# Kernel optimization log

Measured on AMD Instinct MI355X. Metric: run time of the kernel, lower is better.

Reference implementation:

```python
import jax, jax.numpy as jnp
import numpy as np

N_NODES = 50000
N_EDGES = 800000
IN_FEAT = 64
HIDDEN = 128
NUM_LAYERS = 3


def setup_inputs() -> dict:
    key = jax.random.key(0)
    ks = jax.random.split(key, 8)
    x = jax.random.normal(ks[0], (N_NODES, IN_FEAT), dtype=jnp.float32)
    edge_index = jax.random.randint(ks[1], (2, N_EDGES), 0, N_NODES, dtype=jnp.int64)
    s_in = 1.0 / np.sqrt(IN_FEAT)
    s_h = 1.0 / np.sqrt(HIDDEN)
    W_in = jax.random.uniform(ks[2], (IN_FEAT, HIDDEN), jnp.float32, -s_in, s_in)
    b_in = jax.random.uniform(ks[3], (HIDDEN,), jnp.float32, -s_in, s_in)
    W_self = jax.random.uniform(ks[4], (NUM_LAYERS, HIDDEN, HIDDEN), jnp.float32, -s_h, s_h)
    b_self = jax.random.uniform(ks[5], (NUM_LAYERS, HIDDEN), jnp.float32, -s_h, s_h)
    W_nbr = jax.random.uniform(ks[6], (NUM_LAYERS, HIDDEN, HIDDEN), jnp.float32, -s_h, s_h)
    return {"x": x, "edge_index": edge_index, "W_in": W_in, "b_in": b_in,
            "W_self": W_self, "b_self": b_self, "W_nbr": W_nbr}


def reference(x, edge_index, W_in, b_in, W_self, b_self, W_nbr):
    # input projection: h [N, HIDDEN]
    h = x @ W_in + b_in
    src = edge_index[0]
    dst = edge_index[1]
    n = h.shape[0]
    ones = jnp.ones((dst.shape[0], 1), dtype=h.dtype)
    # scatter-mean denominator is grad-constant; compute once
    cnt = jax.ops.segment_sum(ones, dst, num_segments=n)
    cnt = jnp.maximum(cnt, 1.0)
    for l in range(W_self.shape[0]):
        msg = h[src] @ W_nbr[l]                               # [E, HIDDEN]
        agg = jax.ops.segment_sum(msg, dst, num_segments=n) / cnt  # scatter-mean
        h = jax.nn.elu(h @ W_self[l] + b_self[l] + agg)
    return h
```

## Files before the change

kernel.cpp:

```cpp
#include <hip/hip_runtime.h>
#include <cstdint>

#define HIDDEN 128

typedef unsigned short u16;
using frag_t   = __attribute__((ext_vector_type(8))) short;
using f32x4_t  = __attribute__((ext_vector_type(4))) float;
using ushort8_t = __attribute__((ext_vector_type(8))) unsigned short;

__device__ __forceinline__ float bf2f(u16 u) {
    union { unsigned int i; float f; } c;
    c.i = ((unsigned int)u) << 16;
    return c.f;
}
__device__ __forceinline__ u16 f2bf(float f) {
    unsigned int u = __float_as_uint(f);
    unsigned int r = (u + 0x7fffu + ((u >> 16) & 1u)) >> 16;
    return (u16)r;
}


__global__ void k_hist_prep(const int* __restrict__ ei, int E, int* __restrict__ deg, int npr,
                            const float* __restrict__ x,
                            const float* __restrict__ W_in,
                            const float* __restrict__ W_self,
                            const float* __restrict__ W_nbr,
                            u16* __restrict__ xf,
                            u16* __restrict__ WtI_hi, u16* __restrict__ WtI_lo,
                            u16* __restrict__ WtS_hi, u16* __restrict__ WtS_lo,
                            u16* __restrict__ WtN_hi, u16* __restrict__ WtN_lo,
                            int L, int nxg) {
    {
        int r  = blockIdx.x & 7;
        int lo = r * npr, hi = lo + npr;
        int nb = gridDim.x >> 3;
        int bi = blockIdx.x >> 3;
        int tid = bi * blockDim.x + threadIdx.x;
        int stride = nb * blockDim.x;
        if ((E & 3) == 0) {
            const int4* d4 = (const int4*)(ei + E);
            int nch = E >> 2;
            for (int c = tid; c < nch; c += stride) {
                int4 d = d4[c];
                if (d.x >= lo && d.x < hi) atomicAdd(&deg[d.x], 1);
                if (d.y >= lo && d.y < hi) atomicAdd(&deg[d.y], 1);
                if (d.z >= lo && d.z < hi) atomicAdd(&deg[d.z], 1);
                if (d.w >= lo && d.w < hi) atomicAdd(&deg[d.w], 1);
            }
        } else {
            for (int e = tid; e < E; e += stride) {
                int d = ei[E + e];
                if (d >= lo && d < hi) atomicAdd(&deg[d], 1);
            }
        }
    }
    {
        int nIn = 64 * 128;
        int nSq = L * 128 * 128;
        int wtot = nIn + 2 * nSq;
        int total = wtot + nxg;
        int stride = gridDim.x * blockDim.x;
        for (int i = blockIdx.x * blockDim.x + threadIdx.x; i < total; i += stride) {
            if (i >= wtot) {
                int t = i - wtot;
                int row = t >> 3, c = t & 7;
                const float4* xs = (const float4*)(x + (size_t)row * 64 + c * 8);
                float4 v0 = xs[0], v1 = xs[1];
                ushort8_t o;
                o[0] = f2bf(v0.x); o[1] = f2bf(v0.y); o[2] = f2bf(v0.z); o[3] = f2bf(v0.w);
                o[4] = f2bf(v1.x); o[5] = f2bf(v1.y); o[6] = f2bf(v1.z); o[7] = f2bf(v1.w);
                int T = row >> 4, m = row & 15;
                int f = c >> 2, q = c & 3;
                *(ushort8_t*)&xf[((size_t)(T * 2 + f) * 64 + q * 16 + m) * 8] = o;
            } else {
                float v; u16* phi; u16* plo; int o;
                if (i < nIn) {
                    int n = i / 64, k = i % 64;
                    v = W_in[k * 128 + n]; phi = WtI_hi; plo = WtI_lo; o = n * 64 + k;
                } else if (i < nIn + nSq) {
                    int t = i - nIn;
                    int l = t / (128 * 128), r = t % (128 * 128);
                    int n = r / 128, k = r % 128;
                    v = W_self[l * 128 * 128 + k * 128 + n]; phi = WtS_hi; plo = WtS_lo;
                    o = l * 128 * 128 + n * 128 + k;
                } else {
                    int t = i - nIn - nSq;
                    int l = t / (128 * 128), r = t % (128 * 128);
                    int n = r / 128, k = r % 128;
                    v = W_nbr[l * 128 * 128 + k * 128 + n]; phi = WtN_hi; plo = WtN_lo;
                    o = l * 128 * 128 + n * 128 + k;
                }
                u16 hi = f2bf(v);
                phi[o] = hi;
                plo[o] = f2bf(v - bf2f(hi));
            }
        }
    }
}

__global__ void k_scan1(const int* __restrict__ deg, int* __restrict__ rowp,
                        int* __restrict__ bsums, int n) {
    __shared__ int sh[1024];
    int t = threadIdx.x;
    int base = blockIdx.x * 1024;
    int v = (base + t < n) ? deg[base + t] : 0;
    sh[t] = v;
    __syncthreads();
    for (int off = 1; off < 1024; off <<= 1) {
        int x = sh[t];
        int y = (t >= off) ? sh[t - off] : 0;
        __syncthreads();
        sh[t] = x + y;
        __syncthreads();
    }
    if (base + t < n) rowp[base + t + 1] = sh[t];
    if (t == 1023) bsums[blockIdx.x] = sh[1023];
}

__global__ void k_scan_tail(int* __restrict__ rowp, const int* __restrict__ bsums,
                            int* __restrict__ fillp, int n, int nb) {
    __shared__ int sh[1024];
    int t = threadIdx.x;
    int b = blockIdx.x;
    sh[t] = (t < nb) ? bsums[t] : 0;
    __syncthreads();
    for (int off = 1; off < 1024; off <<= 1) {
        int x = sh[t];
        int y = (t >= off) ? sh[t - off] : 0;
        __syncthreads();
        sh[t] = x + y;
        __syncthreads();
    }
    int boff = (b == 0) ? 0 : sh[b - 1];
    int base = b * 1024;
    if (base + t < n) {
        int v = rowp[base + t + 1] + boff;
        rowp[base + t + 1] = v;
        if (base + t + 1 < n) fillp[base + t + 1] = v;
    }
    if (b == 0 && t == 0) { rowp[0] = 0; fillp[0] = 0; }
}

__global__ void k_fill(const int* __restrict__ ei, int E,
                       int* __restrict__ fillpos, int* __restrict__ colx, int npr) {
    int r  = blockIdx.x & 7;
    int lo = r * npr, hi = lo + npr;
    int nb = gridDim.x >> 3;
    int bi = blockIdx.x >> 3;
    int tid = bi * blockDim.x + threadIdx.x;
    int stride = nb * blockDim.x;
    if ((E & 3) == 0) {
        const int4* s4 = (const int4*)ei;
        const int4* d4 = (const int4*)(ei + E);
        int nch = E >> 2;
        for (int c = tid; c < nch; c += stride) {
            int4 d = d4[c];
            bool m0 = d.x >= lo && d.x < hi;
            bool m1 = d.y >= lo && d.y < hi;
            bool m2 = d.z >= lo && d.z < hi;
            bool m3 = d.w >= lo && d.w < hi;
            if (m0 | m1 | m2 | m3) {
                int4 s = s4[c];
                if (m0) colx[atomicAdd(&fillpos[d.x], 1)] = s.x;
                if (m1) colx[atomicAdd(&fillpos[d.y], 1)] = s.y;
                if (m2) colx[atomicAdd(&fillpos[d.z], 1)] = s.z;
                if (m3) colx[atomicAdd(&fillpos[d.w], 1)] = s.w;
            }
        }
    } else {
        for (int e = tid; e < E; e += stride) {
            int d = ei[E + e];
            if (d >= lo && d < hi) colx[atomicAdd(&fillpos[d], 1)] = ei[e];
        }
    }
}


__global__ __launch_bounds__(256, 4) void k_agg(
        const ushort8_t* __restrict__ hb8, const int* __restrict__ rowp,
        const int* __restrict__ colx, u16* __restrict__ Sf, int n) {
    int g = (blockIdx.x * blockDim.x + threadIdx.x) >> 4;
    int lane = threadIdx.x & 15;
    if (g >= n) return;
    int beg = rowp[g];
    int end = rowp[g + 1];
    float a0[8], a1[8];
#pragma unroll
    for (int j = 0; j < 8; ++j) { a0[j] = 0.f; a1[j] = 0.f; }
    int e = beg;
    for (; e + 7 < end; e += 8) {
        int s0 = colx[e],     s1 = colx[e + 1], s2 = colx[e + 2], s3 = colx[e + 3];
        int s4 = colx[e + 4], s5 = colx[e + 5], s6 = colx[e + 6], s7 = colx[e + 7];
        ushort8_t v0 = hb8[(size_t)s0 * 16 + lane];
        ushort8_t v1 = hb8[(size_t)s1 * 16 + lane];
        ushort8_t v2 = hb8[(size_t)s2 * 16 + lane];
        ushort8_t v3 = hb8[(size_t)s3 * 16 + lane];
        ushort8_t v4 = hb8[(size_t)s4 * 16 + lane];
        ushort8_t v5 = hb8[(size_t)s5 * 16 + lane];
        ushort8_t v6 = hb8[(size_t)s6 * 16 + lane];
        ushort8_t v7 = hb8[(size_t)s7 * 16 + lane];
#pragma unroll
        for (int j = 0; j < 8; ++j) {
            a0[j] += bf2f(v0[j]); a1[j] += bf2f(v1[j]);
            a0[j] += bf2f(v2[j]); a1[j] += bf2f(v3[j]);
            a0[j] += bf2f(v4[j]); a1[j] += bf2f(v5[j]);
            a0[j] += bf2f(v6[j]); a1[j] += bf2f(v7[j]);
        }
    }
    for (; e + 3 < end; e += 4) {
        int s0 = colx[e], s1 = colx[e + 1], s2 = colx[e + 2], s3 = colx[e + 3];
        ushort8_t v0 = hb8[(size_t)s0 * 16 + lane];
        ushort8_t v1 = hb8[(size_t)s1 * 16 + lane];
        ushort8_t v2 = hb8[(size_t)s2 * 16 + lane];
        ushort8_t v3 = hb8[(size_t)s3 * 16 + lane];
#pragma unroll
        for (int j = 0; j < 8; ++j) {
            a0[j] += bf2f(v0[j]); a1[j] += bf2f(v1[j]);
            a0[j] += bf2f(v2[j]); a1[j] += bf2f(v3[j]);
        }
    }
    for (; e < end; ++e) {
        int s = colx[e];
        ushort8_t v = hb8[(size_t)s * 16 + lane];
#pragma unroll
        for (int j = 0; j < 8; ++j) a0[j] += bf2f(v[j]);
    }
    int deg = end - beg;
    float inv = 1.0f / (float)(deg > 1 ? deg : 1);
    ushort8_t o;
#pragma unroll
    for (int j = 0; j < 8; ++j) o[j] = f2bf((a0[j] + a1[j]) * inv);
    int T = g >> 4, m = g & 15;
    *(ushort8_t*)&Sf[((size_t)(T * 4 + (lane >> 2)) * 64 + (lane & 3) * 16 + m) * 8] = o;
}


template <int KF1, int KF2, int DO_ELU>
__global__ __launch_bounds__(256, 2) void k_gemm_mfma(
    const u16* __restrict__ A1f, const u16* __restrict__ A2f,
    const u16* __restrict__ B1h, const u16* __restrict__ B1l,
    const u16* __restrict__ B2h, const u16* __restrict__ B2l,
    const float* __restrict__ bias, float* __restrict__ C,
    u16* __restrict__ Hrow, u16* __restrict__ Hf,
    int M)
{
    constexpr int K1 = KF1 * 32;
    constexpr int K2 = KF2 * 32;
    constexpr int KF = KF1 + KF2;
    int lane = threadIdx.x & 63;
    int w    = threadIdx.x >> 6;
    int m16  = lane & 15;
    int quad = lane >> 4;
    int kq   = quad * 8;
    int ng   = (blockIdx.x >> 3) & 1;
    int mtb  = (blockIdx.x & 7) | ((blockIdx.x >> 4) << 3);
    int ncol = (ng * 4 + w) * 16 + m16;

    frag_t bh[KF], bl[KF];
    if constexpr (KF1 > 0) {
#pragma unroll
        for (int f = 0; f < KF1; ++f) {
            bh[f] = *(const frag_t*)&B1h[(size_t)ncol * K1 + f * 32 + kq];
            bl[f] = *(const frag_t*)&B1l[(size_t)ncol * K1 + f * 32 + kq];
        }
    }
    if constexpr (KF2 > 0) {
#pragma unroll
        for (int f = 0; f < KF2; ++f) {
            bh[KF1 + f] = *(const frag_t*)&B2h[(size_t)ncol * K2 + f * 32 + kq];
            bl[KF1 + f] = *(const frag_t*)&B2l[(size_t)ncol * K2 + f * 32 + kq];
        }
    }

    float bv = bias[ncol];
    int nMT  = (M + 31) >> 5;
    int step = gridDim.x >> 1;
    int fcol = ncol >> 5;
    int qcol = (ncol & 31) >> 3;
    int jcol = ncol & 7;

    auto loadA = [&](int mt, frag_t (&a0)[KF], frag_t (&a1)[KF]) {
        int T0 = mt * 2, T1 = T0 + 1;
        if constexpr (KF1 > 0) {
#pragma unroll
            for (int f = 0; f < KF1; ++f) {
                a0[f] = *(const frag_t*)&A1f[((size_t)(T0 * KF1 + f) * 64 + lane) * 8];
                a1[f] = *(const frag_t*)&A1f[((size_t)(T1 * KF1 + f) * 64 + lane) * 8];
            }
        }
        if constexpr (KF2 > 0) {
#pragma unroll
            for (int f = 0; f < KF2; ++f) {
                a0[KF1 + f] = *(const frag_t*)&A2f[((size_t)(T0 * KF2 + f) * 64 + lane) * 8];
                a1[KF1 + f] = *(const frag_t*)&A2f[((size_t)(T1 * KF2 + f) * 64 + lane) * 8];
            }
        }
    };

    auto compute = [&](int mt, frag_t (&a0)[KF], frag_t (&a1)[KF]) {
        f32x4_t acc0 = (f32x4_t){0.f, 0.f, 0.f, 0.f};
        f32x4_t acc1 = (f32x4_t){0.f, 0.f, 0.f, 0.f};
#pragma unroll
        for (int f = 0; f < KF; ++f) {
            acc0 = __builtin_amdgcn_mfma_f32_16x16x32_bf16(a0[f], bh[f], acc0, 0, 0, 0);
            acc1 = __builtin_amdgcn_mfma_f32_16x16x32_bf16(a1[f], bh[f], acc1, 0, 0, 0);
            acc0 = __builtin_amdgcn_mfma_f32_16x16x32_bf16(a0[f], bl[f], acc0, 0, 0, 0);
            acc1 = __builtin_amdgcn_mfma_f32_16x16x32_bf16(a1[f], bl[f], acc1, 0, 0, 0);
        }
        int rb = mt * 32 + quad * 4;
#pragma unroll
        for (int r = 0; r < 4; ++r) {
#pragma unroll
            for (int half = 0; half < 2; ++half) {
                int row = rb + r + half * 16;
                float av = half ? acc1[r] : acc0[r];
                if (row < M) {
                    float v = av + bv;
                    if constexpr (DO_ELU) v = (v > 0.f) ? v : expm1f(v);
                    if (C) C[(size_t)row * HIDDEN + ncol] = v;
                    if (Hrow) {
                        u16 hv = f2bf(v);
                        Hrow[(size_t)row * HIDDEN + ncol] = hv;
                        Hf[((size_t)((row >> 4) * 4 + fcol) * 64 + qcol * 16 + (row & 15)) * 8 + jcol] = hv;
                    }
                }
            }
        }
    };

    int mt = mtb;
    if (mt >= nMT) return;
    frag_t xa0[KF], xa1[KF], ya0[KF], ya1[KF];
    loadA(mt, xa0, xa1);
    while (true) {
        int mt2 = mt + step;
        if (mt2 < nMT) loadA(mt2, ya0, ya1);
        compute(mt, xa0, xa1);
        if (mt2 >= nMT) break;
        int mt3 = mt2 + step;
        if (mt3 < nMT) loadA(mt3, xa0, xa1);
        compute(mt2, ya0, ya1);
        if (mt3 >= nMT) break;
        mt = mt3;
    }
}


extern "C" void kernel_launch(void* const* d_in, const int* in_sizes, int n_in,
                              void* d_out, int out_size, void* d_ws, size_t ws_size,
                              hipStream_t stream) {
    const float* x        = (const float*)d_in[0];
    const int* ei         = (const int*)d_in[1];
    const float* W_in     = (const float*)d_in[2];
    const float* b_in     = (const float*)d_in[3];
    const float* W_self   = (const float*)d_in[4];
    const float* b_self   = (const float*)d_in[5];
    const float* W_nbr    = (const float*)d_in[6];
    float* out = (float*)d_out;

    const int IN_FEAT = 64;
    int N = in_sizes[0] / IN_FEAT;
    int E = in_sizes[1] / 2;
    int L = in_sizes[4] / (HIDDEN * HIDDEN);

    char* ws = (char*)d_ws;
    size_t off = 0;
    auto alloc = [&](size_t bytes) -> void* {
        void* p = ws + off;
        off = (off + bytes + 255) & ~(size_t)255;
        return p;
    };

    int nT = ((N + 31) / 32) * 2;

    u16* hRowA = (u16*)alloc((size_t)N * HIDDEN * 2);
    u16* hRowB = (u16*)alloc((size_t)N * HIDDEN * 2);
    u16* hfA   = (u16*)alloc((size_t)nT * 4 * 64 * 8 * 2);
    u16* hfB   = (u16*)alloc((size_t)nT * 4 * 64 * 8 * 2);
    u16* xf    = (u16*)alloc((size_t)nT * 2 * 64 * 8 * 2);
    u16* Sf    = (u16*)alloc((size_t)nT * 4 * 64 * 8 * 2);
    u16* WtI_hi = (u16*)alloc(128 * 64 * 2);
    u16* WtI_lo = (u16*)alloc(128 * 64 * 2);
    u16* WtS_hi = (u16*)alloc((size_t)L * 128 * 128 * 2);
    u16* WtS_lo = (u16*)alloc((size_t)L * 128 * 128 * 2);
    u16* WtN_hi = (u16*)alloc((size_t)L * 128 * 128 * 2);
    u16* WtN_lo = (u16*)alloc((size_t)L * 128 * 128 * 2);
    int* deg   = (int*)alloc((size_t)N * sizeof(int));
    int* rowp  = (int*)alloc((size_t)(N + 1) * sizeof(int));
    int* fillp = (int*)alloc((size_t)N * sizeof(int));
    int* colx  = (int*)alloc((size_t)E * sizeof(int));
    int* bsums = (int*)alloc(1024 * sizeof(int));

    int npr = (N + 7) / 8;

    hipMemsetAsync(deg, 0, (size_t)N * sizeof(int), stream);
    int wtot = 64 * 128 + 2 * L * 128 * 128;
    k_hist_prep<<<2048, 256, 0, stream>>>(ei, E, deg, npr,
                                          x, W_in, W_self, W_nbr, xf,
                                          WtI_hi, WtI_lo, WtS_hi, WtS_lo,
                                          WtN_hi, WtN_lo, L, N * 8);
    int nb = (N + 1023) / 1024;
    k_scan1<<<nb, 1024, 0, stream>>>(deg, rowp, bsums, N);
    k_scan_tail<<<nb, 1024, 0, stream>>>(rowp, bsums, fillp, N, nb);
    k_fill<<<2048, 256, 0, stream>>>(ei, E, fillp, colx, npr);

    const int GB = 1024;

    k_gemm_mfma<2, 0, 0><<<GB, 256, 0, stream>>>(
        xf, nullptr,
        WtI_hi, WtI_lo, nullptr, nullptr,
        b_in, nullptr, hRowA, hfA, N);

    u16* curRow = hRowA; u16* curF = hfA;
    u16* nxtRow = hRowB; u16* nxtF = hfB;

    for (int l = 0; l < L; ++l) {
        k_agg<<<(N + 15) / 16, 256, 0, stream>>>((const ushort8_t*)curRow, rowp, colx, Sf, N);
        const u16* Wsh = WtS_hi + (size_t)l * 128 * 128;
        const u16* Wsl = WtS_lo + (size_t)l * 128 * 128;
        const u16* Wnh = WtN_hi + (size_t)l * 128 * 128;
        const u16* Wnl = WtN_lo + (size_t)l * 128 * 128;
        const float* bs = b_self + (size_t)l * HIDDEN;
        bool last = (l == L - 1);
        k_gemm_mfma<4, 4, 1><<<GB, 256, 0, stream>>>(
            curF, Sf,
            Wsh, Wsl, Wnh, Wnl,
            bs, last ? out : nullptr,
            last ? nullptr : nxtRow, last ? nullptr : nxtF, N);
        u16* tr = curRow; curRow = nxtRow; nxtRow = tr;
        u16* tf = curF;   curF = nxtF;     nxtF = tf;
    }
}
```

Baseline: 333.1 us.

## Fuse input GEMM and all layer agg/GEMM stages into one persistent kernel

Replaces the separate input-projection GEMM, per-layer aggregation and per-layer GEMM launches with a single persistent kernel of 512 blocks. Stages are separated by an atomic-counter grid barrier, and aggregation becomes a grid-stride loop. This removes the launch overheads and tail gaps between the seven kernels. In exchange it relies on all 512 blocks being co-resident, or the barrier deadlocks. It also changes the GEMM grid from 1024 to 512 blocks, and the aggregation occupancy now follows launch_bounds(256,2) instead of (256,4).

```diff
diff --git a/kernel.cpp b/kernel.cpp
--- a/kernel.cpp
+++ b/kernel.cpp
@@ -17,6 +17,17 @@
     unsigned int u = __float_as_uint(f);
     unsigned int r = (u + 0x7fffu + ((u >> 16) & 1u)) >> 16;
     return (u16)r;
+}
+
+__device__ __forceinline__ void gbar(int* cnt, int target) {
+    __syncthreads();
+    if (threadIdx.x == 0) {
+        __threadfence();
+        __hip_atomic_fetch_add(cnt, 1, __ATOMIC_RELEASE, __HIP_MEMORY_SCOPE_AGENT);
+        while (__hip_atomic_load(cnt, __ATOMIC_ACQUIRE, __HIP_MEMORY_SCOPE_AGENT) < target)
+            __builtin_amdgcn_s_sleep(2);
+    }
+    __syncthreads();
 }
 
 
@@ -176,67 +187,69 @@
 }
 
 
-__global__ __launch_bounds__(256, 4) void k_agg(
-        const ushort8_t* __restrict__ hb8, const int* __restrict__ rowp,
-        const int* __restrict__ colx, u16* __restrict__ Sf, int n) {
-    int g = (blockIdx.x * blockDim.x + threadIdx.x) >> 4;
+__device__ __forceinline__ void dev_agg(const ushort8_t* __restrict__ hb8,
+                                        const int* __restrict__ rowp,
+                                        const int* __restrict__ colx,
+                                        u16* __restrict__ Sf, int n) {
     int lane = threadIdx.x & 15;
-    if (g >= n) return;
-    int beg = rowp[g];
-    int end = rowp[g + 1];
-    float a0[8], a1[8];
-#pragma unroll
-    for (int j = 0; j < 8; ++j) { a0[j] = 0.f; a1[j] = 0.f; }
-    int e = beg;
-    for (; e + 7 < end; e += 8) {
-        int s0 = colx[e],     s1 = colx[e + 1], s2 = colx[e + 2], s3 = colx[e + 3];
-        int s4 = colx[e + 4], s5 = colx[e + 5], s6 = colx[e + 6], s7 = colx[e + 7];
-        ushort8_t v0 = hb8[(size_t)s0 * 16 + lane];
-        ushort8_t v1 = hb8[(size_t)s1 * 16 + lane];
-        ushort8_t v2 = hb8[(size_t)s2 * 16 + lane];
-        ushort8_t v3 = hb8[(size_t)s3 * 16 + lane];
-        ushort8_t v4 = hb8[(size_t)s4 * 16 + lane];
-        ushort8_t v5 = hb8[(size_t)s5 * 16 + lane];
-        ushort8_t v6 = hb8[(size_t)s6 * 16 + lane];
-        ushort8_t v7 = hb8[(size_t)s7 * 16 + lane];
-#pragma unroll
-        for (int j = 0; j < 8; ++j) {
-            a0[j] += bf2f(v0[j]); a1[j] += bf2f(v1[j]);
-            a0[j] += bf2f(v2[j]); a1[j] += bf2f(v3[j]);
-            a0[j] += bf2f(v4[j]); a1[j] += bf2f(v5[j]);
-            a0[j] += bf2f(v6[j]); a1[j] += bf2f(v7[j]);
-        }
-    }
-    for (; e + 3 < end; e += 4) {
-        int s0 = colx[e], s1 = colx[e + 1], s2 = colx[e + 2], s3 = colx[e + 3];
-        ushort8_t v0 = hb8[(size_t)s0 * 16 + lane];
-        ushort8_t v1 = hb8[(size_t)s1 * 16 + lane];
-        ushort8_t v2 = hb8[(size_t)s2 * 16 + lane];
-        ushort8_t v3 = hb8[(size_t)s3 * 16 + lane];
-#pragma unroll
-        for (int j = 0; j < 8; ++j) {
-            a0[j] += bf2f(v0[j]); a1[j] += bf2f(v1[j]);
-            a0[j] += bf2f(v2[j]); a1[j] += bf2f(v3[j]);
-        }
-    }
-    for (; e < end; ++e) {
-        int s = colx[e];
-        ushort8_t v = hb8[(size_t)s * 16 + lane];
-#pragma unroll
-        for (int j = 0; j < 8; ++j) a0[j] += bf2f(v[j]);
-    }
-    int deg = end - beg;
-    float inv = 1.0f / (float)(deg > 1 ? deg : 1);
-    ushort8_t o;
-#pragma unroll
-    for (int j = 0; j < 8; ++j) o[j] = f2bf((a0[j] + a1[j]) * inv);
-    int T = g >> 4, m = g & 15;
-    *(ushort8_t*)&Sf[((size_t)(T * 4 + (lane >> 2)) * 64 + (lane & 3) * 16 + m) * 8] = o;
+    int ngr = (gridDim.x * blockDim.x) >> 4;
+    for (int g = (blockIdx.x * blockDim.x + threadIdx.x) >> 4; g < n; g += ngr) {
+        int beg = rowp[g];
+        int end = rowp[g + 1];
+        float a0[8], a1[8];
+#pragma unroll
+        for (int j = 0; j < 8; ++j) { a0[j] = 0.f; a1[j] = 0.f; }
+        int e = beg;
+        for (; e + 7 < end; e += 8) {
+            int s0 = colx[e],     s1 = colx[e + 1], s2 = colx[e + 2], s3 = colx[e + 3];
+            int s4 = colx[e + 4], s5 = colx[e + 5], s6 = colx[e + 6], s7 = colx[e + 7];
+            ushort8_t v0 = hb8[(size_t)s0 * 16 + lane];
+            ushort8_t v1 = hb8[(size_t)s1 * 16 + lane];
+            ushort8_t v2 = hb8[(size_t)s2 * 16 + lane];
+            ushort8_t v3 = hb8[(size_t)s3 * 16 + lane];
+            ushort8_t v4 = hb8[(size_t)s4 * 16 + lane];
+            ushort8_t v5 = hb8[(size_t)s5 * 16 + lane];
+            ushort8_t v6 = hb8[(size_t)s6 * 16 + lane];
+            ushort8_t v7 = hb8[(size_t)s7 * 16 + lane];
+#pragma unroll
+            for (int j = 0; j < 8; ++j) {
+                a0[j] += bf2f(v0[j]); a1[j] += bf2f(v1[j]);
+                a0[j] += bf2f(v2[j]); a1[j] += bf2f(v3[j]);
+                a0[j] += bf2f(v4[j]); a1[j] += bf2f(v5[j]);
+                a0[j] += bf2f(v6[j]); a1[j] += bf2f(v7[j]);
+            }
+        }
+        for (; e + 3 < end; e += 4) {
+            int s0 = colx[e], s1 = colx[e + 1], s2 = colx[e + 2], s3 = colx[e + 3];
+            ushort8_t v0 = hb8[(size_t)s0 * 16 + lane];
+            ushort8_t v1 = hb8[(size_t)s1 * 16 + lane];
+            ushort8_t v2 = hb8[(size_t)s2 * 16 + lane];
+            ushort8_t v3 = hb8[(size_t)s3 * 16 + lane];
+#pragma unroll
+            for (int j = 0; j < 8; ++j) {
+                a0[j] += bf2f(v0[j]); a1[j] += bf2f(v1[j]);
+                a0[j] += bf2f(v2[j]); a1[j] += bf2f(v3[j]);
+            }
+        }
+        for (; e < end; ++e) {
+            int s = colx[e];
+            ushort8_t v = hb8[(size_t)s * 16 + lane];
+#pragma unroll
+            for (int j = 0; j < 8; ++j) a0[j] += bf2f(v[j]);
+        }
+        int deg = end - beg;
+        float inv = 1.0f / (float)(deg > 1 ? deg : 1);
+        ushort8_t o;
+#pragma unroll
+        for (int j = 0; j < 8; ++j) o[j] = f2bf((a0[j] + a1[j]) * inv);
+        int T = g >> 4, m = g & 15;
+        *(ushort8_t*)&Sf[((size_t)(T * 4 + (lane >> 2)) * 64 + (lane & 3) * 16 + m) * 8] = o;
+    }
 }
 
 
 template <int KF1, int KF2, int DO_ELU>
-__global__ __launch_bounds__(256, 2) void k_gemm_mfma(
+__device__ __forceinline__ void dev_gemm(
     const u16* __restrict__ A1f, const u16* __restrict__ A2f,
     const u16* __restrict__ B1h, const u16* __restrict__ B1l,
     const u16* __restrict__ B2h, const u16* __restrict__ B2l,
@@ -329,19 +342,65 @@
     };
 
     int mt = mtb;
-    if (mt >= nMT) return;
-    frag_t xa0[KF], xa1[KF], ya0[KF], ya1[KF];
-    loadA(mt, xa0, xa1);
-    while (true) {
-        int mt2 = mt + step;
-        if (mt2 < nMT) loadA(mt2, ya0, ya1);
-        compute(mt, xa0, xa1);
-        if (mt2 >= nMT) break;
-        int mt3 = mt2 + step;
-        if (mt3 < nMT) loadA(mt3, xa0, xa1);
-        compute(mt2, ya0, ya1);
-        if (mt3 >= nMT) break;
-        mt = mt3;
+    if (mt < nMT) {
+        frag_t xa0[KF], xa1[KF], ya0[KF], ya1[KF];
+        loadA(mt, xa0, xa1);
+        while (true) {
+            int mt2 = mt + step;
+            if (mt2 < nMT) loadA(mt2, ya0, ya1);
+            compute(mt, xa0, xa1);
+            if (mt2 >= nMT) break;
+            int mt3 = mt2 + step;
+            if (mt3 < nMT) loadA(mt3, xa0, xa1);
+            compute(mt2, ya0, ya1);
+            if (mt3 >= nMT) break;
+            mt = mt3;
+        }
+    }
+}
+
+
+__global__ __launch_bounds__(256, 2) void k_mega(
+    const u16* __restrict__ xf,
+    const u16* __restrict__ WtI_hi, const u16* __restrict__ WtI_lo,
+    const u16* __restrict__ WtS_hi, const u16* __restrict__ WtS_lo,
+    const u16* __restrict__ WtN_hi, const u16* __restrict__ WtN_lo,
+    const float* __restrict__ b_in, const float* __restrict__ b_self,
+    const int* __restrict__ rowp, const int* __restrict__ colx,
+    u16* __restrict__ hRowA, u16* __restrict__ hfA,
+    u16* __restrict__ hRowB, u16* __restrict__ hfB,
+    u16* __restrict__ Sf,
+    float* __restrict__ out,
+    int N, int L, int* __restrict__ cnt)
+{
+    int nb = gridDim.x;
+    int bt = nb;
+
+    dev_gemm<2, 0, 0>(xf, nullptr, WtI_hi, WtI_lo, nullptr, nullptr,
+                      b_in, nullptr, hRowA, hfA, N);
+    gbar(cnt, bt); bt += nb;
+
+    u16* curRow = hRowA; u16* curF = hfA;
+    u16* nxtRow = hRowB; u16* nxtF = hfB;
+
+    for (int l = 0; l < L; ++l) {
+        dev_agg((const ushort8_t*)curRow, rowp, colx, Sf, N);
+        gbar(cnt, bt); bt += nb;
+
+        const u16* Wsh = WtS_hi + (size_t)l * 128 * 128;
+        const u16* Wsl = WtS_lo + (size_t)l * 128 * 128;
+        const u16* Wnh = WtN_hi + (size_t)l * 128 * 128;
+        const u16* Wnl = WtN_lo + (size_t)l * 128 * 128;
+        const float* bs = b_self + (size_t)l * HIDDEN;
+        bool last = (l == L - 1);
+        dev_gemm<4, 4, 1>(curF, Sf, Wsh, Wsl, Wnh, Wnl, bs,
+                          last ? out : nullptr,
+                          last ? nullptr : nxtRow, last ? nullptr : nxtF, N);
+        if (!last) {
+            gbar(cnt, bt); bt += nb;
+            u16* tr = curRow; curRow = nxtRow; nxtRow = tr;
+            u16* tf = curF;   curF = nxtF;     nxtF = tf;
+        }
     }
 }
 
@@ -385,7 +444,8 @@
     u16* WtS_lo = (u16*)alloc((size_t)L * 128 * 128 * 2);
     u16* WtN_hi = (u16*)alloc((size_t)L * 128 * 128 * 2);
     u16* WtN_lo = (u16*)alloc((size_t)L * 128 * 128 * 2);
-    int* deg   = (int*)alloc((size_t)N * sizeof(int));
+    int* deg   = (int*)alloc((size_t)(N + 64) * sizeof(int));
+    int* cnt   = deg + N;
     int* rowp  = (int*)alloc((size_t)(N + 1) * sizeof(int));
     int* fillp = (int*)alloc((size_t)N * sizeof(int));
     int* colx  = (int*)alloc((size_t)E * sizeof(int));
@@ -393,8 +453,7 @@
 
     int npr = (N + 7) / 8;
 
-    hipMemsetAsync(deg, 0, (size_t)N * sizeof(int), stream);
-    int wtot = 64 * 128 + 2 * L * 128 * 128;
+    hipMemsetAsync(deg, 0, (size_t)(N + 64) * sizeof(int), stream);
     k_hist_prep<<<2048, 256, 0, stream>>>(ei, E, deg, npr,
                                           x, W_in, W_self, W_nbr, xf,
                                           WtI_hi, WtI_lo, WtS_hi, WtS_lo,
@@ -404,30 +463,8 @@
     k_scan_tail<<<nb, 1024, 0, stream>>>(rowp, bsums, fillp, N, nb);
     k_fill<<<2048, 256, 0, stream>>>(ei, E, fillp, colx, npr);
 
-    const int GB = 1024;
-
-    k_gemm_mfma<2, 0, 0><<<GB, 256, 0, stream>>>(
-        xf, nullptr,
-        WtI_hi, WtI_lo, nullptr, nullptr,
-        b_in, nullptr, hRowA, hfA, N);
-
-    u16* curRow = hRowA; u16* curF = hfA;
-    u16* nxtRow = hRowB; u16* nxtF = hfB;
-
-    for (int l = 0; l < L; ++l) {
-        k_agg<<<(N + 15) / 16, 256, 0, stream>>>((const ushort8_t*)curRow, rowp, colx, Sf, N);
-        const u16* Wsh = WtS_hi + (size_t)l * 128 * 128;
-        const u16* Wsl = WtS_lo + (size_t)l * 128 * 128;
-        const u16* Wnh = WtN_hi + (size_t)l * 128 * 128;
-        const u16* Wnl = WtN_lo + (size_t)l * 128 * 128;
-        const float* bs = b_self + (size_t)l * HIDDEN;
-        bool last = (l == L - 1);
-        k_gemm_mfma<4, 4, 1><<<GB, 256, 0, stream>>>(
-            curF, Sf,
-            Wsh, Wsl, Wnh, Wnl,
-            bs, last ? out : nullptr,
-            last ? nullptr : nxtRow, last ? nullptr : nxtF, N);
-        u16* tr = curRow; curRow = nxtRow; nxtRow = tr;
-        u16* tf = curF;   curF = nxtF;     nxtF = tf;
-    }
-}
+    k_mega<<<512, 256, 0, stream>>>(
+        xf, WtI_hi, WtI_lo, WtS_hi, WtS_lo, WtN_hi, WtN_lo,
+        b_in, b_self, rowp, colx,
+        hRowA, hfA, hRowB, hfB, Sf, out, N, L, cnt);
+}
```

New measurement: 815.7 us. 2.45x slower.

## Drop fragment-layout copies; GEMM reads row-major activations and converts x inline

Applied to the files above, without the earlier changes.

The pre-swizzled MFMA fragment buffers (xf, hf, Sf) are removed. The GEMM now loads A operands directly from row-major bf16 activations, and for the input projection it reads fp32 x and converts it to bf16 in registers, which eliminates the x conversion pass in the prep kernel and the duplicate fragment-layout store in the epilogue. The aggregation kernel writes S row-major and gains a 16-edge unrolled gather loop for more memory-level parallelism. The trade-off is that row-major fragment loads are strided per lane rather than fully contiguous, so GEMM load efficiency may drop.

```diff
diff --git a/kernel.cpp b/kernel.cpp
--- a/kernel.cpp
+++ b/kernel.cpp
@@ -20,16 +20,14 @@
 }
 
 
-__global__ void k_hist_prep(const int* __restrict__ ei, int E, int* __restrict__ deg, int npr,
-                            const float* __restrict__ x,
-                            const float* __restrict__ W_in,
-                            const float* __restrict__ W_self,
-                            const float* __restrict__ W_nbr,
-                            u16* __restrict__ xf,
-                            u16* __restrict__ WtI_hi, u16* __restrict__ WtI_lo,
-                            u16* __restrict__ WtS_hi, u16* __restrict__ WtS_lo,
-                            u16* __restrict__ WtN_hi, u16* __restrict__ WtN_lo,
-                            int L, int nxg) {
+__global__ void k_hist_wprep(const int* __restrict__ ei, int E, int* __restrict__ deg, int npr,
+                             const float* __restrict__ W_in,
+                             const float* __restrict__ W_self,
+                             const float* __restrict__ W_nbr,
+                             u16* __restrict__ WtI_hi, u16* __restrict__ WtI_lo,
+                             u16* __restrict__ WtS_hi, u16* __restrict__ WtS_lo,
+                             u16* __restrict__ WtN_hi, u16* __restrict__ WtN_lo,
+                             int L) {
     {
         int r  = blockIdx.x & 7;
         int lo = r * npr, hi = lo + npr;
@@ -58,42 +56,28 @@
         int nIn = 64 * 128;
         int nSq = L * 128 * 128;
         int wtot = nIn + 2 * nSq;
-        int total = wtot + nxg;
         int stride = gridDim.x * blockDim.x;
-        for (int i = blockIdx.x * blockDim.x + threadIdx.x; i < total; i += stride) {
-            if (i >= wtot) {
-                int t = i - wtot;
-                int row = t >> 3, c = t & 7;
-                const float4* xs = (const float4*)(x + (size_t)row * 64 + c * 8);
-                float4 v0 = xs[0], v1 = xs[1];
-                ushort8_t o;
-                o[0] = f2bf(v0.x); o[1] = f2bf(v0.y); o[2] = f2bf(v0.z); o[3] = f2bf(v0.w);
-                o[4] = f2bf(v1.x); o[5] = f2bf(v1.y); o[6] = f2bf(v1.z); o[7] = f2bf(v1.w);
-                int T = row >> 4, m = row & 15;
-                int f = c >> 2, q = c & 3;
-                *(ushort8_t*)&xf[((size_t)(T * 2 + f) * 64 + q * 16 + m) * 8] = o;
+        for (int i = blockIdx.x * blockDim.x + threadIdx.x; i < wtot; i += stride) {
+            float v; u16* phi; u16* plo; int o;
+            if (i < nIn) {
+                int n = i / 64, k = i % 64;
+                v = W_in[k * 128 + n]; phi = WtI_hi; plo = WtI_lo; o = n * 64 + k;
+            } else if (i < nIn + nSq) {
+                int t = i - nIn;
+                int l = t / (128 * 128), r = t % (128 * 128);
+                int n = r / 128, k = r % 128;
+                v = W_self[l * 128 * 128 + k * 128 + n]; phi = WtS_hi; plo = WtS_lo;
+                o = l * 128 * 128 + n * 128 + k;
             } else {
-                float v; u16* phi; u16* plo; int o;
-                if (i < nIn) {
-                    int n = i / 64, k = i % 64;
-                    v = W_in[k * 128 + n]; phi = WtI_hi; plo = WtI_lo; o = n * 64 + k;
-                } else if (i < nIn + nSq) {
-                    int t = i - nIn;
-                    int l = t / (128 * 128), r = t % (128 * 128);
-                    int n = r / 128, k = r % 128;
-                    v = W_self[l * 128 * 128 + k * 128 + n]; phi = WtS_hi; plo = WtS_lo;
-                    o = l * 128 * 128 + n * 128 + k;
-                } else {
-                    int t = i - nIn - nSq;
-                    int l = t / (128 * 128), r = t % (128 * 128);
-                    int n = r / 128, k = r % 128;
-                    v = W_nbr[l * 128 * 128 + k * 128 + n]; phi = WtN_hi; plo = WtN_lo;
-                    o = l * 128 * 128 + n * 128 + k;
-                }
-                u16 hi = f2bf(v);
-                phi[o] = hi;
-                plo[o] = f2bf(v - bf2f(hi));
-            }
+                int t = i - nIn - nSq;
+                int l = t / (128 * 128), r = t % (128 * 128);
+                int n = r / 128, k = r % 128;
+                v = W_nbr[l * 128 * 128 + k * 128 + n]; phi = WtN_hi; plo = WtN_lo;
+                o = l * 128 * 128 + n * 128 + k;
+            }
+            u16 hi = f2bf(v);
+            phi[o] = hi;
+            plo[o] = f2bf(v - bf2f(hi));
         }
     }
 }
@@ -178,7 +162,7 @@
 
 __global__ __launch_bounds__(256, 4) void k_agg(
         const ushort8_t* __restrict__ hb8, const int* __restrict__ rowp,
-        const int* __restrict__ colx, u16* __restrict__ Sf, int n) {
+        const int* __restrict__ colx, u16* __restrict__ S, int n) {
     int g = (blockIdx.x * blockDim.x + threadIdx.x) >> 4;
     int lane = threadIdx.x & 15;
     if (g >= n) return;
@@ -188,6 +172,42 @@
 #pragma unroll
     for (int j = 0; j < 8; ++j) { a0[j] = 0.f; a1[j] = 0.f; }
     int e = beg;
+    for (; e + 15 < end; e += 16) {
+        int s0 = colx[e],      s1 = colx[e + 1],  s2 = colx[e + 2],  s3 = colx[e + 3];
+        int s4 = colx[e + 4],  s5 = colx[e + 5],  s6 = colx[e + 6],  s7 = colx[e + 7];
+        int s8 = colx[e + 8],  s9 = colx[e + 9],  sa = colx[e + 10], sb = colx[e + 11];
+        int sc = colx[e + 12], sd = colx[e + 13], se = colx[e + 14], sf = colx[e + 15];
+        ushort8_t v0 = hb8[(size_t)s0 * 16 + lane];
+        ushort8_t v1 = hb8[(size_t)s1 * 16 + lane];
+        ushort8_t v2 = hb8[(size_t)s2 * 16 + lane];
+        ushort8_t v3 = hb8[(size_t)s3 * 16 + lane];
+        ushort8_t v4 = hb8[(size_t)s4 * 16 + lane];
+        ushort8_t v5 = hb8[(size_t)s5 * 16 + lane];
+        ushort8_t v6 = hb8[(size_t)s6 * 16 + lane];
+        ushort8_t v7 = hb8[(size_t)s7 * 16 + lane];
+        ushort8_t v8 = hb8[(size_t)s8 * 16 + lane];
+        ushort8_t v9 = hb8[(size_t)s9 * 16 + lane];
+        ushort8_t va = hb8[(size_t)sa * 16 + lane];
+        ushort8_t vb = hb8[(size_t)sb * 16 + lane];
+        ushort8_t vc = hb8[(size_t)sc * 16 + lane];
+        ushort8_t vd = hb8[(size_t)sd * 16 + lane];
+        ushort8_t ve = hb8[(size_t)se * 16 + lane];
+        ushort8_t vf = hb8[(size_t)sf * 16 + lane];
+#pragma unroll
+        for (int j = 0; j < 8; ++j) {
+            a0[j] += bf2f(v0[j]); a1[j] += bf2f(v1[j]);
+            a0[j] += bf2f(v2[j]); a1[j] += bf2f(v3[j]);
+            a0[j] += bf2f(v4[j]); a1[j] += bf2f(v5[j]);
+            a0[j] += bf2f(v6[j]); a1[j] += bf2f(v7[j]);
+        }
+#pragma unroll
+        for (int j = 0; j < 8; ++j) {
+            a0[j] += bf2f(v8[j]); a1[j] += bf2f(v9[j]);
+            a0[j] += bf2f(va[j]); a1[j] += bf2f(vb[j]);
+            a0[j] += bf2f(vc[j]); a1[j] += bf2f(vd[j]);
+            a0[j] += bf2f(ve[j]); a1[j] += bf2f(vf[j]);
+        }
+    }
     for (; e + 7 < end; e += 8) {
         int s0 = colx[e],     s1 = colx[e + 1], s2 = colx[e + 2], s3 = colx[e + 3];
         int s4 = colx[e + 4], s5 = colx[e + 5], s6 = colx[e + 6], s7 = colx[e + 7];
@@ -230,23 +250,23 @@
     ushort8_t o;
 #pragma unroll
     for (int j = 0; j < 8; ++j) o[j] = f2bf((a0[j] + a1[j]) * inv);
-    int T = g >> 4, m = g & 15;
-    *(ushort8_t*)&Sf[((size_t)(T * 4 + (lane >> 2)) * 64 + (lane & 3) * 16 + m) * 8] = o;
-}
-
-
-template <int KF1, int KF2, int DO_ELU>
+    *(ushort8_t*)&S[(size_t)g * 128 + lane * 8] = o;
+}
+
+
+template <int KF1, int KF2, int DO_ELU, int A1F32>
 __global__ __launch_bounds__(256, 2) void k_gemm_mfma(
-    const u16* __restrict__ A1f, const u16* __restrict__ A2f,
+    const void* __restrict__ A1v, const u16* __restrict__ A2,
     const u16* __restrict__ B1h, const u16* __restrict__ B1l,
     const u16* __restrict__ B2h, const u16* __restrict__ B2l,
     const float* __restrict__ bias, float* __restrict__ C,
-    u16* __restrict__ Hrow, u16* __restrict__ Hf,
-    int M)
+    u16* __restrict__ Hrow, int M)
 {
     constexpr int K1 = KF1 * 32;
     constexpr int K2 = KF2 * 32;
     constexpr int KF = KF1 + KF2;
+    const u16*   A1b = (const u16*)A1v;
+    const float* A1x = (const float*)A1v;
     int lane = threadIdx.x & 63;
     int w    = threadIdx.x >> 6;
     int m16  = lane & 15;
@@ -275,24 +295,46 @@
     float bv = bias[ncol];
     int nMT  = (M + 31) >> 5;
     int step = gridDim.x >> 1;
-    int fcol = ncol >> 5;
-    int qcol = (ncol & 31) >> 3;
-    int jcol = ncol & 7;
 
     auto loadA = [&](int mt, frag_t (&a0)[KF], frag_t (&a1)[KF]) {
-        int T0 = mt * 2, T1 = T0 + 1;
+        int r0 = mt * 32 + m16;
+        int r1 = r0 + 16;
+        r0 = r0 < M ? r0 : M - 1;
+        r1 = r1 < M ? r1 : M - 1;
         if constexpr (KF1 > 0) {
-#pragma unroll
-            for (int f = 0; f < KF1; ++f) {
-                a0[f] = *(const frag_t*)&A1f[((size_t)(T0 * KF1 + f) * 64 + lane) * 8];
-                a1[f] = *(const frag_t*)&A1f[((size_t)(T1 * KF1 + f) * 64 + lane) * 8];
+            if constexpr (A1F32) {
+#pragma unroll
+                for (int f = 0; f < KF1; ++f) {
+                    const float* p0 = A1x + (size_t)r0 * K1 + f * 32 + kq;
+                    const float* p1 = A1x + (size_t)r1 * K1 + f * 32 + kq;
+                    float4 u0 = *(const float4*)p0;
+                    float4 u1 = *(const float4*)(p0 + 4);
+                    float4 w0 = *(const float4*)p1;
+                    float4 w1 = *(const float4*)(p1 + 4);
+                    frag_t t0, t1;
+                    t0[0] = (short)f2bf(u0.x); t0[1] = (short)f2bf(u0.y);
+                    t0[2] = (short)f2bf(u0.z); t0[3] = (short)f2bf(u0.w);
+                    t0[4] = (short)f2bf(u1.x); t0[5] = (short)f2bf(u1.y);
+                    t0[6] = (short)f2bf(u1.z); t0[7] = (short)f2bf(u1.w);
+                    t1[0] = (short)f2bf(w0.x); t1[1] = (short)f2bf(w0.y);
+                    t1[2] = (short)f2bf(w0.z); t1[3] = (short)f2bf(w0.w);
+                    t1[4] = (short)f2bf(w1.x); t1[5] = (short)f2bf(w1.y);
+                    t1[6] = (short)f2bf(w1.z); t1[7] = (short)f2bf(w1.w);
+                    a0[f] = t0; a1[f] = t1;
+                }
+            } else {
+#pragma unroll
+                for (int f = 0; f < KF1; ++f) {
+                    a0[f] = *(const frag_t*)&A1b[(size_t)r0 * K1 + f * 32 + kq];
+                    a1[f] = *(const frag_t*)&A1b[(size_t)r1 * K1 + f * 32 + kq];
+                }
             }
         }
         if constexpr (KF2 > 0) {
 #pragma unroll
             for (int f = 0; f < KF2; ++f) {
-                a0[KF1 + f] = *(const frag_t*)&A2f[((size_t)(T0 * KF2 + f) * 64 + lane) * 8];
-                a1[KF1 + f] = *(const frag_t*)&A2f[((size_t)(T1 * KF2 + f) * 64 + lane) * 8];
+                a0[KF1 + f] = *(const frag_t*)&A2[(size_t)r0 * K2 + f * 32 + kq];
+                a1[KF1 + f] = *(const frag_t*)&A2[(size_t)r1 * K2 + f * 32 + kq];
             }
         }
     };
@@ -318,11 +360,7 @@
                     float v = av + bv;
                     if constexpr (DO_ELU) v = (v > 0.f) ? v : expm1f(v);
                     if (C) C[(size_t)row * HIDDEN + ncol] = v;
-                    if (Hrow) {
-                        u16 hv = f2bf(v);
-                        Hrow[(size_t)row * HIDDEN + ncol] = hv;
-                        Hf[((size_t)((row >> 4) * 4 + fcol) * 64 + qcol * 16 + (row & 15)) * 8 + jcol] = hv;
-                    }
+                    if (Hrow) Hrow[(size_t)row * HIDDEN + ncol] = f2bf(v);
                 }
             }
         }
@@ -371,14 +409,9 @@
         return p;
     };
 
-    int nT = ((N + 31) / 32) * 2;
-
-    u16* hRowA = (u16*)alloc((size_t)N * HIDDEN * 2);
-    u16* hRowB = (u16*)alloc((size_t)N * HIDDEN * 2);
-    u16* hfA   = (u16*)alloc((size_t)nT * 4 * 64 * 8 * 2);
-    u16* hfB   = (u16*)alloc((size_t)nT * 4 * 64 * 8 * 2);
-    u16* xf    = (u16*)alloc((size_t)nT * 2 * 64 * 8 * 2);
-    u16* Sf    = (u16*)alloc((size_t)nT * 4 * 64 * 8 * 2);
+    u16* hRowA = (u16*)alloc((size_t)(N + 32) * HIDDEN * 2);
+    u16* hRowB = (u16*)alloc((size_t)(N + 32) * HIDDEN * 2);
+    u16* S     = (u16*)alloc((size_t)(N + 32) * HIDDEN * 2);
     u16* WtI_hi = (u16*)alloc(128 * 64 * 2);
     u16* WtI_lo = (u16*)alloc(128 * 64 * 2);
     u16* WtS_hi = (u16*)alloc((size_t)L * 128 * 128 * 2);
@@ -394,11 +427,10 @@
     int npr = (N + 7) / 8;
 
     hipMemsetAsync(deg, 0, (size_t)N * sizeof(int), stream);
-    int wtot = 64 * 128 + 2 * L * 128 * 128;
-    k_hist_prep<<<2048, 256, 0, stream>>>(ei, E, deg, npr,
-                                          x, W_in, W_self, W_nbr, xf,
-                                          WtI_hi, WtI_lo, WtS_hi, WtS_lo,
-                                          WtN_hi, WtN_lo, L, N * 8);
+    k_hist_wprep<<<2048, 256, 0, stream>>>(ei, E, deg, npr,
+                                           W_in, W_self, W_nbr,
+                                           WtI_hi, WtI_lo, WtS_hi, WtS_lo,
+                                           WtN_hi, WtN_lo, L);
     int nb = (N + 1023) / 1024;
     k_scan1<<<nb, 1024, 0, stream>>>(deg, rowp, bsums, N);
     k_scan_tail<<<nb, 1024, 0, stream>>>(rowp, bsums, fillp, N, nb);
@@ -406,28 +438,27 @@
 
     const int GB = 1024;
 
-    k_gemm_mfma<2, 0, 0><<<GB, 256, 0, stream>>>(
-        xf, nullptr,
+    k_gemm_mfma<2, 0, 0, 1><<<GB, 256, 0, stream>>>(
+        x, nullptr,
         WtI_hi, WtI_lo, nullptr, nullptr,
-        b_in, nullptr, hRowA, hfA, N);
-
-    u16* curRow = hRowA; u16* curF = hfA;
-    u16* nxtRow = hRowB; u16* nxtF = hfB;
+        b_in, nullptr, hRowA, N);
+
+    u16* curRow = hRowA;
+    u16* nxtRow = hRowB;
 
     for (int l = 0; l < L; ++l) {
-        k_agg<<<(N + 15) / 16, 256, 0, stream>>>((const ushort8_t*)curRow, rowp, colx, Sf, N);
+        k_agg<<<(N + 15) / 16, 256, 0, stream>>>((const ushort8_t*)curRow, rowp, colx, S, N);
         const u16* Wsh = WtS_hi + (size_t)l * 128 * 128;
         const u16* Wsl = WtS_lo + (size_t)l * 128 * 128;
         const u16* Wnh = WtN_hi + (size_t)l * 128 * 128;
         const u16* Wnl = WtN_lo + (size_t)l * 128 * 128;
         const float* bs = b_self + (size_t)l * HIDDEN;
         bool last = (l == L - 1);
-        k_gemm_mfma<4, 4, 1><<<GB, 256, 0, stream>>>(
-            curF, Sf,
+        k_gemm_mfma<4, 4, 1, 0><<<GB, 256, 0, stream>>>(
+            curRow, S,
             Wsh, Wsl, Wnh, Wnl,
             bs, last ? out : nullptr,
-            last ? nullptr : nxtRow, last ? nullptr : nxtF, N);
+            last ? nullptr : nxtRow, N);
         u16* tr = curRow; curRow = nxtRow; nxtRow = tr;
-        u16* tf = curF;   curF = nxtF;     nxtF = tf;
-    }
-}
+    }
+}
```

After: 379.4 us. 13.9% more time.

## Fuse CSR fill with input-projection GEMM and unroll aggregation by sixteen

Applied to the files above, without the earlier changes.

Merges the independent CSR fill kernel and the input-projection GEMM into one launch whose blocks are split by index, so the atomic-bound fill and the MFMA GEMM can run at the same time and one launch is saved. It also adds a 16-edge unrolled gather loop in the aggregation kernel to keep more loads in flight per lane. The fused kernel takes the GEMM's launch bounds, which may change register allocation for the fill path, and the wider unroll raises register pressure in the aggregation kernel.

```diff
diff --git a/kernel.cpp b/kernel.cpp
--- a/kernel.cpp
+++ b/kernel.cpp
@@ -141,12 +141,14 @@
     if (b == 0 && t == 0) { rowp[0] = 0; fillp[0] = 0; }
 }
 
-__global__ void k_fill(const int* __restrict__ ei, int E,
-                       int* __restrict__ fillpos, int* __restrict__ colx, int npr) {
-    int r  = blockIdx.x & 7;
+
+__device__ __forceinline__ void dev_fill(const int* __restrict__ ei, int E,
+                                         int* __restrict__ fillpos, int* __restrict__ colx,
+                                         int npr, int bid, int nbF) {
+    int r  = bid & 7;
     int lo = r * npr, hi = lo + npr;
-    int nb = gridDim.x >> 3;
-    int bi = blockIdx.x >> 3;
+    int nb = nbF >> 3;
+    int bi = bid >> 3;
     int tid = bi * blockDim.x + threadIdx.x;
     int stride = nb * blockDim.x;
     if ((E & 3) == 0) {
@@ -188,6 +190,42 @@
 #pragma unroll
     for (int j = 0; j < 8; ++j) { a0[j] = 0.f; a1[j] = 0.f; }
     int e = beg;
+    for (; e + 15 < end; e += 16) {
+        int s0 = colx[e],      s1 = colx[e + 1],  s2 = colx[e + 2],  s3 = colx[e + 3];
+        int s4 = colx[e + 4],  s5 = colx[e + 5],  s6 = colx[e + 6],  s7 = colx[e + 7];
+        int s8 = colx[e + 8],  s9 = colx[e + 9],  sa = colx[e + 10], sb = colx[e + 11];
+        int sc = colx[e + 12], sd = colx[e + 13], se = colx[e + 14], sf = colx[e + 15];
+        ushort8_t v0 = hb8[(size_t)s0 * 16 + lane];
+        ushort8_t v1 = hb8[(size_t)s1 * 16 + lane];
+        ushort8_t v2 = hb8[(size_t)s2 * 16 + lane];
+        ushort8_t v3 = hb8[(size_t)s3 * 16 + lane];
+        ushort8_t v4 = hb8[(size_t)s4 * 16 + lane];
+        ushort8_t v5 = hb8[(size_t)s5 * 16 + lane];
+        ushort8_t v6 = hb8[(size_t)s6 * 16 + lane];
+        ushort8_t v7 = hb8[(size_t)s7 * 16 + lane];
+        ushort8_t v8 = hb8[(size_t)s8 * 16 + lane];
+        ushort8_t v9 = hb8[(size_t)s9 * 16 + lane];
+        ushort8_t va = hb8[(size_t)sa * 16 + lane];
+        ushort8_t vb = hb8[(size_t)sb * 16 + lane];
+        ushort8_t vc = hb8[(size_t)sc * 16 + lane];
+        ushort8_t vd = hb8[(size_t)sd * 16 + lane];
+        ushort8_t ve = hb8[(size_t)se * 16 + lane];
+        ushort8_t vf = hb8[(size_t)sf * 16 + lane];
+#pragma unroll
+        for (int j = 0; j < 8; ++j) {
+            a0[j] += bf2f(v0[j]); a1[j] += bf2f(v1[j]);
+            a0[j] += bf2f(v2[j]); a1[j] += bf2f(v3[j]);
+            a0[j] += bf2f(v4[j]); a1[j] += bf2f(v5[j]);
+            a0[j] += bf2f(v6[j]); a1[j] += bf2f(v7[j]);
+        }
+#pragma unroll
+        for (int j = 0; j < 8; ++j) {
+            a0[j] += bf2f(v8[j]); a1[j] += bf2f(v9[j]);
+            a0[j] += bf2f(va[j]); a1[j] += bf2f(vb[j]);
+            a0[j] += bf2f(vc[j]); a1[j] += bf2f(vd[j]);
+            a0[j] += bf2f(ve[j]); a1[j] += bf2f(vf[j]);
+        }
+    }
     for (; e + 7 < end; e += 8) {
         int s0 = colx[e],     s1 = colx[e + 1], s2 = colx[e + 2], s3 = colx[e + 3];
         int s4 = colx[e + 4], s5 = colx[e + 5], s6 = colx[e + 6], s7 = colx[e + 7];
@@ -236,13 +274,13 @@
 
 
 template <int KF1, int KF2, int DO_ELU>
-__global__ __launch_bounds__(256, 2) void k_gemm_mfma(
+__device__ __forceinline__ void dev_gemm(
     const u16* __restrict__ A1f, const u16* __restrict__ A2f,
     const u16* __restrict__ B1h, const u16* __restrict__ B1l,
     const u16* __restrict__ B2h, const u16* __restrict__ B2l,
     const float* __restrict__ bias, float* __restrict__ C,
     u16* __restrict__ Hrow, u16* __restrict__ Hf,
-    int M)
+    int M, int bid, int gdim)
 {
     constexpr int K1 = KF1 * 32;
     constexpr int K2 = KF2 * 32;
@@ -252,8 +290,8 @@
     int m16  = lane & 15;
     int quad = lane >> 4;
     int kq   = quad * 8;
-    int ng   = (blockIdx.x >> 3) & 1;
-    int mtb  = (blockIdx.x & 7) | ((blockIdx.x >> 4) << 3);
+    int ng   = (bid >> 3) & 1;
+    int mtb  = (bid & 7) | ((bid >> 4) << 3);
     int ncol = (ng * 4 + w) * 16 + m16;
 
     frag_t bh[KF], bl[KF];
@@ -274,7 +312,7 @@
 
     float bv = bias[ncol];
     int nMT  = (M + 31) >> 5;
-    int step = gridDim.x >> 1;
+    int step = gdim >> 1;
     int fcol = ncol >> 5;
     int qcol = (ncol & 31) >> 3;
     int jcol = ncol & 7;
@@ -329,19 +367,49 @@
     };
 
     int mt = mtb;
-    if (mt >= nMT) return;
-    frag_t xa0[KF], xa1[KF], ya0[KF], ya1[KF];
-    loadA(mt, xa0, xa1);
-    while (true) {
-        int mt2 = mt + step;
-        if (mt2 < nMT) loadA(mt2, ya0, ya1);
-        compute(mt, xa0, xa1);
-        if (mt2 >= nMT) break;
-        int mt3 = mt2 + step;
-        if (mt3 < nMT) loadA(mt3, xa0, xa1);
-        compute(mt2, ya0, ya1);
-        if (mt3 >= nMT) break;
-        mt = mt3;
+    if (mt < nMT) {
+        frag_t xa0[KF], xa1[KF], ya0[KF], ya1[KF];
+        loadA(mt, xa0, xa1);
+        while (true) {
+            int mt2 = mt + step;
+            if (mt2 < nMT) loadA(mt2, ya0, ya1);
+            compute(mt, xa0, xa1);
+            if (mt2 >= nMT) break;
+            int mt3 = mt2 + step;
+            if (mt3 < nMT) loadA(mt3, xa0, xa1);
+            compute(mt2, ya0, ya1);
+            if (mt3 >= nMT) break;
+            mt = mt3;
+        }
+    }
+}
+
+template <int KF1, int KF2, int DO_ELU>
+__global__ __launch_bounds__(256, 2) void k_gemm_mfma(
+    const u16* __restrict__ A1f, const u16* __restrict__ A2f,
+    const u16* __restrict__ B1h, const u16* __restrict__ B1l,
+    const u16* __restrict__ B2h, const u16* __restrict__ B2l,
+    const float* __restrict__ bias, float* __restrict__ C,
+    u16* __restrict__ Hrow, u16* __restrict__ Hf, int M)
+{
+    dev_gemm<KF1, KF2, DO_ELU>(A1f, A2f, B1h, B1l, B2h, B2l, bias, C, Hrow, Hf,
+                               M, blockIdx.x, gridDim.x);
+}
+
+
+__global__ __launch_bounds__(256, 2) void k_fill_gemm(
+    const int* __restrict__ ei, int E, int* __restrict__ fillpos, int* __restrict__ colx,
+    int npr, int nbF,
+    const u16* __restrict__ xf,
+    const u16* __restrict__ WtI_hi, const u16* __restrict__ WtI_lo,
+    const float* __restrict__ b_in,
+    u16* __restrict__ hRow, u16* __restrict__ hf, int M, int gdim)
+{
+    if (blockIdx.x < (unsigned)nbF) {
+        dev_fill(ei, E, fillpos, colx, npr, blockIdx.x, nbF);
+    } else {
+        dev_gemm<2, 0, 0>(xf, nullptr, WtI_hi, WtI_lo, nullptr, nullptr,
+                          b_in, nullptr, hRow, hf, M, blockIdx.x - nbF, gdim);
     }
 }
 
@@ -395,6 +463,7 @@
 
     hipMemsetAsync(deg, 0, (size_t)N * sizeof(int), stream);
     int wtot = 64 * 128 + 2 * L * 128 * 128;
+    (void)wtot;
     k_hist_prep<<<2048, 256, 0, stream>>>(ei, E, deg, npr,
                                           x, W_in, W_self, W_nbr, xf,
                                           WtI_hi, WtI_lo, WtS_hi, WtS_lo,
@@ -402,14 +471,13 @@
     int nb = (N + 1023) / 1024;
     k_scan1<<<nb, 1024, 0, stream>>>(deg, rowp, bsums, N);
     k_scan_tail<<<nb, 1024, 0, stream>>>(rowp, bsums, fillp, N, nb);
-    k_fill<<<2048, 256, 0, stream>>>(ei, E, fillp, colx, npr);
 
     const int GB = 1024;
-
-    k_gemm_mfma<2, 0, 0><<<GB, 256, 0, stream>>>(
-        xf, nullptr,
-        WtI_hi, WtI_lo, nullptr, nullptr,
-        b_in, nullptr, hRowA, hfA, N);
+    const int NBF = 2048;
+
+    k_fill_gemm<<<NBF + GB, 256, 0, stream>>>(
+        ei, E, fillp, colx, npr, NBF,
+        xf, WtI_hi, WtI_lo, b_in, hRowA, hfA, N, GB);
 
     u16* curRow = hRowA; u16* curF = hfA;
     u16* nxtRow = hRowB; u16* nxtF = hfB;
```

Measured after the change: 326.7 us. Within noise of the previous version (-1.9%).
